# Performance work log

Hardware: AMD Instinct MI355X
Metric: run time of the kernel (lower is better)

## Reference

```python
import jax, jax.numpy as jnp
import numpy as np

N_BEST = 50          # hypotheses per utterance segment
NUM_SEG = 1_000_000  # number of utterance segments
TOTAL = N_BEST * NUM_SEG


def setup_inputs() -> dict:
    key = jax.random.key(0)
    scores = jax.random.normal(key, (TOTAL,), dtype=jnp.float32)
    # per-segment n-best counts; sum(nBestIndex) == len(scores)
    nBestIndex = jnp.full((NUM_SEG,), N_BEST, dtype=jnp.int32)
    return {"scores": scores, "nBestIndex": nBestIndex}


def reference(scores, nBestIndex):
    # Segmented (ragged) softmax: softmax within each contiguous n-best group.
    # Equivalent to the torch loop with log_score=False, fused into one pass.
    num_seg = nBestIndex.shape[0]
    total = scores.shape[0]
    # segment id for each score element
    seg = jnp.repeat(jnp.arange(num_seg, dtype=jnp.int32), nBestIndex,
                     total_repeat_length=total)
    # numerically stable segmented softmax
    seg_max = jax.ops.segment_max(scores, seg, num_segments=num_seg)
    exps = jnp.exp(scores - seg_max[seg])
    seg_sum = jax.ops.segment_sum(exps, seg, num_segments=num_seg)
    return exps / seg_sum[seg]
```

## Files before the change

kernel.cpp:

```cpp
#include <hip/hip_runtime.h>
#include <math.h>


#define GSEG 16
#define SBLOCK 256
#define SEG_PER_BLOCK (SBLOCK / GSEG)

__global__ __launch_bounds__(256) void scan_local_kernel(
    const int* __restrict__ counts, int n_seg,
    int* __restrict__ local_scan, int* __restrict__ block_sums) {
    __shared__ int sm[256];
    const int t = threadIdx.x;
    const int g = blockIdx.x * 256 + t;
    const int v = (g < n_seg) ? counts[g] : 0;
    sm[t] = v;
    __syncthreads();
    for (int off = 1; off < 256; off <<= 1) {
        int y = (t >= off) ? sm[t - off] : 0;
        __syncthreads();
        sm[t] += y;
        __syncthreads();
    }
    if (g < n_seg) local_scan[g] = sm[t] - v;
    if (t == 255) block_sums[blockIdx.x] = sm[255];
}

__global__ __launch_bounds__(256) void scan_bsums_kernel(
    int* __restrict__ bsum, int nb) {
    __shared__ int sm[256];
    const int t = threadIdx.x;
    const int per = (nb + 255) >> 8;
    const int beg = t * per;
    const int end = (beg + per < nb) ? beg + per : nb;
    int tot = 0;
    for (int j = beg; j < end; ++j) tot += bsum[j];
    sm[t] = tot;
    __syncthreads();
    for (int off = 1; off < 256; off <<= 1) {
        int y = (t >= off) ? sm[t - off] : 0;
        __syncthreads();
        sm[t] += y;
        __syncthreads();
    }
    int run = sm[t] - tot;
    for (int j = beg; j < end; ++j) {
        int v = bsum[j];
        bsum[j] = run;
        run += v;
    }
}

__global__ __launch_bounds__(SBLOCK) void seg_softmax_kernel(
    const float* __restrict__ scores,
    const int* __restrict__ local_scan, const int* __restrict__ bsum,
    float* __restrict__ out, int n_seg, int total) {
    const int tid = threadIdx.x;
    const int p   = tid & (GSEG - 1);
    const int seg = blockIdx.x * SEG_PER_BLOCK + (tid >> 4);
    if (seg >= n_seg) return;

    const int st = local_scan[seg] + bsum[seg >> 8];
    int en;
    if (seg + 1 < n_seg) en = local_scan[seg + 1] + bsum[(seg + 1) >> 8];
    else                 en = total;
    const int c = en - st;
    if (c <= 0) return;

    if (c <= 4 * GSEG) {
        const int i0 = p, i1 = p + GSEG, i2 = p + 2 * GSEG, i3 = p + 3 * GSEG;
        float v0 = -INFINITY, v1 = -INFINITY, v2 = -INFINITY, v3 = -INFINITY;
        if (i0 < c) v0 = scores[st + i0];
        if (i1 < c) v1 = scores[st + i1];
        if (i2 < c) v2 = scores[st + i2];
        if (i3 < c) v3 = scores[st + i3];

        float m = fmaxf(fmaxf(v0, v1), fmaxf(v2, v3));
        #pragma unroll
        for (int off = 1; off < GSEG; off <<= 1)
            m = fmaxf(m, __shfl_xor(m, off, GSEG));

        v0 = __expf(v0 - m);
        v1 = __expf(v1 - m);
        v2 = __expf(v2 - m);
        v3 = __expf(v3 - m);
        float s = (v0 + v1) + (v2 + v3);
        #pragma unroll
        for (int off = 1; off < GSEG; off <<= 1)
            s += __shfl_xor(s, off, GSEG);

        const float inv = 1.0f / s;
        if (i0 < c) out[st + i0] = v0 * inv;
        if (i1 < c) out[st + i1] = v1 * inv;
        if (i2 < c) out[st + i2] = v2 * inv;
        if (i3 < c) out[st + i3] = v3 * inv;
    } else {
        float m = -INFINITY;
        for (int j = p; j < c; j += GSEG)
            m = fmaxf(m, scores[st + j]);
        #pragma unroll
        for (int off = 1; off < GSEG; off <<= 1)
            m = fmaxf(m, __shfl_xor(m, off, GSEG));

        float s = 0.0f;
        for (int j = p; j < c; j += GSEG)
            s += __expf(scores[st + j] - m);
        #pragma unroll
        for (int off = 1; off < GSEG; off <<= 1)
            s += __shfl_xor(s, off, GSEG);

        const float inv = 1.0f / s;
        for (int j = p; j < c; j += GSEG)
            out[st + j] = __expf(scores[st + j] - m) * inv;
    }
}

extern "C" void kernel_launch(void* const* d_in, const int* in_sizes, int n_in,
                              void* d_out, int out_size, void* d_ws, size_t ws_size,
                              hipStream_t stream) {
    const float* scores = (const float*)d_in[0];
    const int*   counts = (const int*)d_in[1];
    float* out = (float*)d_out;
    const int n_seg = in_sizes[1];
    const int total = in_sizes[0];

    int* local_scan = (int*)d_ws;
    const int nblocksA = (n_seg + 255) / 256;
    int* block_sums = local_scan + n_seg;

    scan_local_kernel<<<nblocksA, 256, 0, stream>>>(counts, n_seg, local_scan, block_sums);
    scan_bsums_kernel<<<1, 256, 0, stream>>>(block_sums, nblocksA);

    const int nblocksC = (n_seg + SEG_PER_BLOCK - 1) / SEG_PER_BLOCK;
    seg_softmax_kernel<<<nblocksC, SBLOCK, 0, stream>>>(
        scores, local_scan, block_sums, out, n_seg, total);
}
```

Measured before the change: 352.9 us.

## Process four segments per 16-lane group with shared-memory segment starts

Each 16-thread group now handles four segments instead of one, so a block covers 64 segments and the grid shrinks fourfold. Segment start offsets are loaded once per block into shared memory, so each offset is read only once instead of twice from global memory. All loads for the four segments are issued before any reduction, which raises memory-level parallelism per thread. The division is replaced by the hardware reciprocal approximation, at the cost of a little precision, higher register use and a block-wide barrier.

```diff
diff --git a/kernel.cpp b/kernel.cpp
--- a/kernel.cpp
+++ b/kernel.cpp
@@ -2,9 +2,10 @@
 #include <math.h>
 
 
-#define GSEG 16
+#define GSEG   16
+#define SPG    4
 #define SBLOCK 256
-#define SEG_PER_BLOCK (SBLOCK / GSEG)
+#define SEGS_B ((SBLOCK / GSEG) * SPG)
 
 __global__ __launch_bounds__(256) void scan_local_kernel(
     const int* __restrict__ counts, int n_seg,
@@ -54,63 +55,88 @@
     const float* __restrict__ scores,
     const int* __restrict__ local_scan, const int* __restrict__ bsum,
     float* __restrict__ out, int n_seg, int total) {
-    const int tid = threadIdx.x;
+    __shared__ int starts[SEGS_B + 1];
+
+    const int tid  = threadIdx.x;
+    const int seg0 = blockIdx.x * SEGS_B;
+
+    if (tid <= SEGS_B) {
+        const int s = seg0 + tid;
+        starts[tid] = (s < n_seg) ? (local_scan[s] + bsum[s >> 8]) : total;
+    }
+    __syncthreads();
+
     const int p   = tid & (GSEG - 1);
-    const int seg = blockIdx.x * SEG_PER_BLOCK + (tid >> 4);
-    if (seg >= n_seg) return;
+    const int grp = tid >> 4;
 
-    const int st = local_scan[seg] + bsum[seg >> 8];
-    int en;
-    if (seg + 1 < n_seg) en = local_scan[seg + 1] + bsum[(seg + 1) >> 8];
-    else                 en = total;
-    const int c = en - st;
-    if (c <= 0) return;
+    int st[SPG], c[SPG];
+    #pragma unroll
+    for (int q = 0; q < SPG; ++q) {
+        const int ls = grp * SPG + q;
+        st[q] = starts[ls];
+        c[q]  = starts[ls + 1] - st[q];
+    }
 
-    if (c <= 4 * GSEG) {
-        const int i0 = p, i1 = p + GSEG, i2 = p + 2 * GSEG, i3 = p + 3 * GSEG;
-        float v0 = -INFINITY, v1 = -INFINITY, v2 = -INFINITY, v3 = -INFINITY;
-        if (i0 < c) v0 = scores[st + i0];
-        if (i1 < c) v1 = scores[st + i1];
-        if (i2 < c) v2 = scores[st + i2];
-        if (i3 < c) v3 = scores[st + i3];
+    bool all_small = true;
+    #pragma unroll
+    for (int q = 0; q < SPG; ++q) all_small &= (c[q] <= 4 * GSEG);
 
-        float m = fmaxf(fmaxf(v0, v1), fmaxf(v2, v3));
+    if (all_small) {
+        float v[SPG][4];
         #pragma unroll
-        for (int off = 1; off < GSEG; off <<= 1)
-            m = fmaxf(m, __shfl_xor(m, off, GSEG));
+        for (int q = 0; q < SPG; ++q) {
+            #pragma unroll
+            for (int r = 0; r < 4; ++r) {
+                const int idx = p + r * GSEG;
+                v[q][r] = (idx < c[q]) ? scores[st[q] + idx] : -INFINITY;
+            }
+        }
 
-        v0 = __expf(v0 - m);
-        v1 = __expf(v1 - m);
-        v2 = __expf(v2 - m);
-        v3 = __expf(v3 - m);
-        float s = (v0 + v1) + (v2 + v3);
         #pragma unroll
-        for (int off = 1; off < GSEG; off <<= 1)
-            s += __shfl_xor(s, off, GSEG);
+        for (int q = 0; q < SPG; ++q) {
+            if (c[q] <= 0) continue;
+            float m = fmaxf(fmaxf(v[q][0], v[q][1]), fmaxf(v[q][2], v[q][3]));
+            #pragma unroll
+            for (int off = 1; off < GSEG; off <<= 1)
+                m = fmaxf(m, __shfl_xor(m, off, GSEG));
 
-        const float inv = 1.0f / s;
-        if (i0 < c) out[st + i0] = v0 * inv;
-        if (i1 < c) out[st + i1] = v1 * inv;
-        if (i2 < c) out[st + i2] = v2 * inv;
-        if (i3 < c) out[st + i3] = v3 * inv;
+            const float e0 = __expf(v[q][0] - m);
+            const float e1 = __expf(v[q][1] - m);
+            const float e2 = __expf(v[q][2] - m);
+            const float e3 = __expf(v[q][3] - m);
+            float s = (e0 + e1) + (e2 + e3);
+            #pragma unroll
+            for (int off = 1; off < GSEG; off <<= 1)
+                s += __shfl_xor(s, off, GSEG);
+
+            const float inv = __builtin_amdgcn_rcpf(s);
+            if (p < c[q])             out[st[q] + p]            = e0 * inv;
+            if (p + GSEG < c[q])      out[st[q] + p + GSEG]     = e1 * inv;
+            if (p + 2 * GSEG < c[q])  out[st[q] + p + 2 * GSEG] = e2 * inv;
+            if (p + 3 * GSEG < c[q])  out[st[q] + p + 3 * GSEG] = e3 * inv;
+        }
     } else {
-        float m = -INFINITY;
-        for (int j = p; j < c; j += GSEG)
-            m = fmaxf(m, scores[st + j]);
         #pragma unroll
-        for (int off = 1; off < GSEG; off <<= 1)
-            m = fmaxf(m, __shfl_xor(m, off, GSEG));
+        for (int q = 0; q < SPG; ++q) {
+            if (c[q] <= 0) continue;
+            float m = -INFINITY;
+            for (int j = p; j < c[q]; j += GSEG)
+                m = fmaxf(m, scores[st[q] + j]);
+            #pragma unroll
+            for (int off = 1; off < GSEG; off <<= 1)
+                m = fmaxf(m, __shfl_xor(m, off, GSEG));
 
-        float s = 0.0f;
-        for (int j = p; j < c; j += GSEG)
-            s += __expf(scores[st + j] - m);
-        #pragma unroll
-        for (int off = 1; off < GSEG; off <<= 1)
-            s += __shfl_xor(s, off, GSEG);
+            float s = 0.0f;
+            for (int j = p; j < c[q]; j += GSEG)
+                s += __expf(scores[st[q] + j] - m);
+            #pragma unroll
+            for (int off = 1; off < GSEG; off <<= 1)
+                s += __shfl_xor(s, off, GSEG);
 
-        const float inv = 1.0f / s;
-        for (int j = p; j < c; j += GSEG)
-            out[st + j] = __expf(scores[st + j] - m) * inv;
+            const float inv = __builtin_amdgcn_rcpf(s);
+            for (int j = p; j < c[q]; j += GSEG)
+                out[st[q] + j] = __expf(scores[st[q] + j] - m) * inv;
+        }
     }
 }
 
@@ -130,7 +156,7 @@
     scan_local_kernel<<<nblocksA, 256, 0, stream>>>(counts, n_seg, local_scan, block_sums);
     scan_bsums_kernel<<<1, 256, 0, stream>>>(block_sums, nblocksA);
 
-    const int nblocksC = (n_seg + SEG_PER_BLOCK - 1) / SEG_PER_BLOCK;
+    const int nblocksC = (n_seg + SEGS_B - 1) / SEGS_B;
     seg_softmax_kernel<<<nblocksC, SBLOCK, 0, stream>>>(
         scores, local_scan, block_sums, out, n_seg, total);
 }
```

Measured after the change: 364.7 us. +3.4%, slower.
